# Kernel optimization log

Hardware: AMD Instinct MI355X
Metric: run time of the kernel (lower is better)

## Reference

```python
import jax, jax.numpy as jnp
import numpy as np

B, L, ENC_DIM, DEC_DIM, ATTN_DIM = 64, 2048, 1024, 1024, 512


def setup_inputs() -> dict:
    key = jax.random.key(0)
    ks = jax.random.split(key, 8)
    s_enc = 1.0 / np.sqrt(ENC_DIM)
    s_dec = 1.0 / np.sqrt(DEC_DIM)
    s_full = 1.0 / np.sqrt(ATTN_DIM)
    return {
        "encoder_out": jax.random.normal(ks[0], (B, L, ENC_DIM), jnp.float32),
        "decoder_hidden": jax.random.normal(ks[1], (B, DEC_DIM), jnp.float32),
        "We_w": jax.random.uniform(ks[2], (ENC_DIM, ATTN_DIM), jnp.float32, -s_enc, s_enc),
        "We_b": jax.random.uniform(ks[3], (ATTN_DIM,), jnp.float32, -s_enc, s_enc),
        "Wd_w": jax.random.uniform(ks[4], (DEC_DIM, ATTN_DIM), jnp.float32, -s_dec, s_dec),
        "Wd_b": jax.random.uniform(ks[5], (ATTN_DIM,), jnp.float32, -s_dec, s_dec),
        "Wf_w": jax.random.uniform(ks[6], (ATTN_DIM,), jnp.float32, -s_full, s_full),
        "Wf_b": jax.random.uniform(ks[7], (), jnp.float32, -s_full, s_full),
    }


def reference(encoder_out, decoder_hidden, We_w, We_b, Wd_w, Wd_b, Wf_w, Wf_b):
    # enc_attn: [B, L, A]; dec_attn: [B, A]
    enc_attn = jnp.einsum("ble,ea->bla", encoder_out, We_w) + We_b
    dec_attn = decoder_hidden @ Wd_w + Wd_b
    # additive score -> scalar per (B, L)
    hidden = jax.nn.relu(enc_attn + dec_attn[:, None, :])
    attn = jnp.einsum("bla,a->bl", hidden, Wf_w) + Wf_b
    alpha = jax.nn.softmax(attn, axis=1)  # over sequence dim
    weighted = jnp.einsum("ble,bl->be", encoder_out, alpha)
    return (weighted, alpha)
```

## Files before the change

kernel.cpp:

```cpp
#include <hip/hip_runtime.h>
#include <stdint.h>

#define B_BATCH 64
#define L_SEQ 2048
#define E_DIM 1024
#define A_DIM 512

typedef __attribute__((ext_vector_type(4))) float f32x4;
typedef __attribute__((ext_vector_type(8))) short bf16x8;
typedef __attribute__((ext_vector_type(2))) unsigned int u32x2;
typedef __attribute__((ext_vector_type(4))) unsigned int u32x4;

__device__ __forceinline__ unsigned short f2bf(float f) {
  unsigned u = __float_as_uint(f);
  u = (u + 0x7fffu + ((u >> 16) & 1u)) >> 16;
  return (unsigned short)u;
}

__device__ __forceinline__ u32x2 packbf(f32x4 v) {
  u32x2 r;
  r.x = (unsigned)f2bf(v.x) | ((unsigned)f2bf(v.y) << 16);
  r.y = (unsigned)f2bf(v.z) | ((unsigned)f2bf(v.w) << 16);
  return r;
}

#define CHUNKB 8192
#define ABUF (4 * CHUNKB)
#define BCHUNK 32768
#define BCOPY (32 * BCHUNK)

__global__ void prep_we_kernel(const float* __restrict__ We, char* __restrict__ wsB) {
  int t = blockIdx.x * 256 + threadIdx.x;
  int lane = t & 63;
  int colblk = (t >> 6) & 31;
  int step = t >> 11;
  int nl = lane & 15, g = lane >> 4;
  int col = colblk * 16 + nl;
  int k0 = step * 32 + 4 * g;
  unsigned q0 = (unsigned)f2bf(We[(size_t)(k0 + 0) * A_DIM + col]) |
                ((unsigned)f2bf(We[(size_t)(k0 + 1) * A_DIM + col]) << 16);
  unsigned q1 = (unsigned)f2bf(We[(size_t)(k0 + 2) * A_DIM + col]) |
                ((unsigned)f2bf(We[(size_t)(k0 + 3) * A_DIM + col]) << 16);
  unsigned q2 = (unsigned)f2bf(We[(size_t)(k0 + 16) * A_DIM + col]) |
                ((unsigned)f2bf(We[(size_t)(k0 + 17) * A_DIM + col]) << 16);
  unsigned q3 = (unsigned)f2bf(We[(size_t)(k0 + 18) * A_DIM + col]) |
                ((unsigned)f2bf(We[(size_t)(k0 + 19) * A_DIM + col]) << 16);
  u32x4 v; v.x = q0; v.y = q1; v.z = q2; v.w = q3;
#pragma unroll
  for (int c = 0; c < 8; ++c)
    *(u32x4*)(wsB + (size_t)c * BCOPY + (size_t)t * 16) = v;
}

__global__ void dec_comb_kernel(const float* __restrict__ dh, const float* __restrict__ Wd,
                                const float* __restrict__ Wdb, const float* __restrict__ Web,
                                float* __restrict__ dcomb) {
  __shared__ float sh[1024];
  const int b = blockIdx.x, tid = threadIdx.x;
  for (int i = tid; i < 1024; i += 128) sh[i] = dh[b * 1024 + i];
  __syncthreads();
  const int a = blockIdx.y * 128 + tid;
  float acc = Wdb[a] + Web[a];
#pragma unroll 4
  for (int e = 0; e < 1024; ++e) acc += sh[e] * Wd[(size_t)e * A_DIM + a];
  dcomb[b * A_DIM + a] = acc;
}

__global__ __launch_bounds__(512, 2) void score_gemm_kernel(
    const float* __restrict__ enc, const char* __restrict__ wsB,
    const float* __restrict__ dcomb, const float* __restrict__ wf,
    float* __restrict__ scoreOut) {
  __shared__ __align__(16) char smem[2 * ABUF];
  __shared__ float s_score[128];

  const int tid = threadIdx.x;
  const int lane = tid & 63;
  const int w = tid >> 6;
  const int g = lane >> 4;
  const int nl = lane & 15;
  const int gs = g ^ ((nl >> 1) & 3);

  const int row0 = (int)blockIdx.x * 128;
  const int bb = row0 >> 11;

  if (tid < 128) s_score[tid] = 0.0f;

  const float* encA = enc + (size_t)row0 * E_DIM;
  const int anl = nl * 64 + gs * 16;

  const int arow = tid >> 5;
  const int klq = tid & 31;
  const float* asrc = encA + (size_t)arow * E_DIM + klq * 4;
  const int aw_base = (klq >> 3) * CHUNKB + arow * 64 +
                      (((tid & 3) ^ ((arow >> 1) & 3)) << 4) + ((tid >> 2) & 1) * 8;

  const char* bsrc = wsB + (size_t)(blockIdx.x & 7) * BCOPY + (w * 4) * 1024 + lane * 16;

  f32x4 acc[8][4];
#pragma unroll
  for (int rt = 0; rt < 8; ++rt)
#pragma unroll
    for (int ct = 0; ct < 4; ++ct) {
      f32x4 z = {0.f, 0.f, 0.f, 0.f};
      acc[rt][ct] = z;
    }
  f32x4 ra[2][2];
  bf16x8 bfr[2][4];

#define LOAD_P(t_, s_)                                                          \
  do {                                                                          \
    ra[(s_) & 1][0] =                                                           \
        *(const f32x4*)(asrc + (size_t)(2 * (s_)) * 16 * E_DIM + (t_) * 128);   \
    ra[(s_) & 1][1] =                                                           \
        *(const f32x4*)(asrc + (size_t)(2 * (s_) + 1) * 16 * E_DIM + (t_) * 128); \
  } while (0)

#define LOAD_B(kcg_, sl_)                                                       \
  do {                                                                          \
    _Pragma("unroll") for (int ct = 0; ct < 4; ++ct) bfr[sl_][ct] =             \
        *(const bf16x8*)(bsrc + (size_t)(kcg_)*BCHUNK + ct * 1024);             \
  } while (0)

#define WRITE_P(s_, nb_)                                                        \
  do {                                                                          \
    *(u32x2*)(smem + (nb_) + aw_base + (2 * (s_)) * 1024) = packbf(ra[(s_) & 1][0]); \
    *(u32x2*)(smem + (nb_) + aw_base + (2 * (s_) + 1) * 1024) =                 \
        packbf(ra[(s_) & 1][1]);                                                \
  } while (0)

#define MFMA_CHUNK(cb_, s_, par_)                                               \
  do {                                                                          \
    bf16x8 afr[4];                                                              \
    _Pragma("unroll") for (int rt = 0; rt < 4; ++rt) afr[rt] =                  \
        *(const bf16x8*)(smem + (cb_) + (s_)*CHUNKB + anl + rt * 1024);         \
    __builtin_amdgcn_s_setprio(1);                                              \
    _Pragma("unroll") for (int rt = 0; rt < 4; ++rt)                            \
        _Pragma("unroll") for (int ct = 0; ct < 4; ++ct) acc[rt][ct] =          \
            __builtin_amdgcn_mfma_f32_16x16x32_bf16(afr[rt], bfr[par_][ct],     \
                                                    acc[rt][ct], 0, 0, 0);      \
    __builtin_amdgcn_s_setprio(0);                                              \
    _Pragma("unroll") for (int rt = 0; rt < 4; ++rt) afr[rt] =                  \
        *(const bf16x8*)(smem + (cb_) + (s_)*CHUNKB + anl + (rt + 4) * 1024);   \
    __builtin_amdgcn_s_setprio(1);                                              \
    _Pragma("unroll") for (int rt = 0; rt < 4; ++rt)                            \
        _Pragma("unroll") for (int ct = 0; ct < 4; ++ct) acc[rt + 4][ct] =      \
            __builtin_amdgcn_mfma_f32_16x16x32_bf16(afr[rt], bfr[par_][ct],     \
                                                    acc[rt + 4][ct], 0, 0, 0);  \
    __builtin_amdgcn_s_setprio(0);                                              \
  } while (0)

  LOAD_P(0, 0);
  LOAD_P(0, 1);
  asm volatile("s_waitcnt vmcnt(2)" ::: "memory");
  WRITE_P(0, 0);
  LOAD_P(0, 2);
  asm volatile("s_waitcnt vmcnt(2)" ::: "memory");
  WRITE_P(1, 0);
  LOAD_P(0, 3);
  asm volatile("s_waitcnt vmcnt(2)" ::: "memory");
  WRITE_P(2, 0);
  asm volatile("s_waitcnt vmcnt(0)" ::: "memory");
  WRITE_P(3, 0);
  LOAD_B(0, 0);
  asm volatile("s_waitcnt lgkmcnt(0)" ::: "memory");
  asm volatile("s_barrier" ::: "memory");

#pragma unroll 1
  for (int t = 0; t < 7; ++t) {
    const int cb = (t & 1) * ABUF;
    const int nb = cb ^ ABUF;
    LOAD_P(t + 1, 0);
    LOAD_B(4 * t + 1, 1);
    asm volatile("s_waitcnt vmcnt(6)" ::: "memory");
    MFMA_CHUNK(cb, 0, 0);
    LOAD_P(t + 1, 1);
    LOAD_B(4 * t + 2, 0);
    asm volatile("s_waitcnt vmcnt(6)" ::: "memory");
    WRITE_P(0, nb);
    MFMA_CHUNK(cb, 1, 1);
    LOAD_P(t + 1, 2);
    LOAD_B(4 * t + 3, 1);
    asm volatile("s_waitcnt vmcnt(6)" ::: "memory");
    WRITE_P(1, nb);
    MFMA_CHUNK(cb, 2, 0);
    LOAD_P(t + 1, 3);
    LOAD_B(4 * t + 4, 0);
    asm volatile("s_waitcnt vmcnt(4)" ::: "memory");
    WRITE_P(2, nb);
    WRITE_P(3, nb);
    MFMA_CHUNK(cb, 3, 1);
    asm volatile("s_waitcnt lgkmcnt(0)" ::: "memory");
    asm volatile("s_barrier" ::: "memory");
  }
  {
    const int cb = ABUF;
    LOAD_B(29, 1);
    asm volatile("s_waitcnt vmcnt(4)" ::: "memory");
    MFMA_CHUNK(cb, 0, 0);
    LOAD_B(30, 0);
    asm volatile("s_waitcnt vmcnt(4)" ::: "memory");
    MFMA_CHUNK(cb, 1, 1);
    LOAD_B(31, 1);
    asm volatile("s_waitcnt vmcnt(4)" ::: "memory");
    MFMA_CHUNK(cb, 2, 0);
    asm volatile("s_waitcnt vmcnt(0)" ::: "memory");
    MFMA_CHUNK(cb, 3, 1);
  }

#undef LOAD_P
#undef LOAD_B
#undef WRITE_P
#undef MFMA_CHUNK

  float db[4], wv[4];
#pragma unroll
  for (int ct = 0; ct < 4; ++ct) {
    int a = w * 64 + ct * 16 + nl;
    db[ct] = dcomb[bb * A_DIM + a];
    wv[ct] = wf[a];
  }
#pragma unroll
  for (int rt = 0; rt < 8; ++rt) {
#pragma unroll
    for (int r = 0; r < 4; ++r) {
      float p = 0.f;
#pragma unroll
      for (int ct = 0; ct < 4; ++ct) {
        float h = acc[rt][ct][r] + db[ct];
        h = h > 0.f ? h : 0.f;
        p += h * wv[ct];
      }
      p += __shfl_xor(p, 1);
      p += __shfl_xor(p, 2);
      p += __shfl_xor(p, 4);
      p += __shfl_xor(p, 8);
      if (nl == 0) atomicAdd(&s_score[rt * 16 + g * 4 + r], p);
    }
  }
  __syncthreads();
  if (tid < 128) scoreOut[row0 + tid] = s_score[tid];
}

__global__ void softmax_kernel(float* __restrict__ attn) {
  __shared__ float red[8];
  const int b = blockIdx.x, tid = threadIdx.x;
  float* p = attn + b * L_SEQ;
  float v[8];
  float m = -1e30f;
#pragma unroll
  for (int i = 0; i < 8; ++i) {
    v[i] = p[tid + i * 256];
    m = fmaxf(m, v[i]);
  }
#pragma unroll
  for (int off = 1; off < 64; off <<= 1) m = fmaxf(m, __shfl_xor(m, off));
  const int wid = tid >> 6;
  if ((tid & 63) == 0) red[wid] = m;
  __syncthreads();
  m = fmaxf(fmaxf(red[0], red[1]), fmaxf(red[2], red[3]));
  float s = 0.f;
#pragma unroll
  for (int i = 0; i < 8; ++i) {
    v[i] = __expf(v[i] - m);
    s += v[i];
  }
#pragma unroll
  for (int off = 1; off < 64; off <<= 1) s += __shfl_xor(s, off);
  __syncthreads();
  if ((tid & 63) == 0) red[4 + wid] = s;
  __syncthreads();
  const float inv = 1.0f / (red[4] + red[5] + red[6] + red[7]);
#pragma unroll
  for (int i = 0; i < 8; ++i) p[tid + i * 256] = v[i] * inv;
}

__global__ void weighted_part_kernel(const float* __restrict__ enc,
                                     const float* __restrict__ alpha,
                                     float* __restrict__ part) {
  __shared__ float sa[64];
  const int bid = blockIdx.x;
  const int b = bid >> 5, ls = bid & 31;
  const int tid = threadIdx.x;
  if (tid < 64) sa[tid] = alpha[b * L_SEQ + ls * 64 + tid];
  __syncthreads();
  const float* base = enc + ((size_t)(b * L_SEQ + ls * 64)) * E_DIM;
  f32x4 acc = {0.f, 0.f, 0.f, 0.f};
#pragma unroll 8
  for (int il = 0; il < 64; ++il) {
    f32x4 v = *(const f32x4*)(base + (size_t)il * E_DIM + tid * 4);
    float al = sa[il];
    acc.x += al * v.x;
    acc.y += al * v.y;
    acc.z += al * v.z;
    acc.w += al * v.w;
  }
  *(f32x4*)(part + (size_t)bid * E_DIM + tid * 4) = acc;
}

__global__ void weighted_reduce_kernel(const float* __restrict__ part,
                                       float* __restrict__ outW) {
  const int b = blockIdx.x, tid = threadIdx.x;
  const float* p = part + (size_t)b * 32 * E_DIM + tid * 4;
  f32x4 acc = {0.f, 0.f, 0.f, 0.f};
#pragma unroll 8
  for (int ls = 0; ls < 32; ++ls) {
    f32x4 v = *(const f32x4*)(p + (size_t)ls * E_DIM);
    acc.x += v.x;
    acc.y += v.y;
    acc.z += v.z;
    acc.w += v.w;
  }
  *(f32x4*)(outW + (size_t)b * E_DIM + tid * 4) = acc;
}

extern "C" void kernel_launch(void* const* d_in, const int* in_sizes, int n_in,
                              void* d_out, int out_size, void* d_ws, size_t ws_size,
                              hipStream_t stream) {
  const float* enc = (const float*)d_in[0];
  const float* dh = (const float*)d_in[1];
  const float* WeW = (const float*)d_in[2];
  const float* WeB = (const float*)d_in[3];
  const float* WdW = (const float*)d_in[4];
  const float* WdB = (const float*)d_in[5];
  const float* WfW = (const float*)d_in[6];

  float* out = (float*)d_out;
  float* outW = out;
  float* attn = out + B_BATCH * E_DIM;

  char* wsB = (char*)d_ws;
  float* dcomb = (float*)((char*)d_ws + 8 * (size_t)BCOPY);
  float* part = (float*)((char*)d_ws + 8 * (size_t)BCOPY +
                         (size_t)B_BATCH * A_DIM * sizeof(float));

  const size_t need = 8 * (size_t)BCOPY + (size_t)B_BATCH * A_DIM * sizeof(float) +
                      (size_t)B_BATCH * 32 * E_DIM * sizeof(float);
  if (ws_size < need) return;

  prep_we_kernel<<<256, 256, 0, stream>>>(WeW, wsB);
  dec_comb_kernel<<<dim3(B_BATCH, 4), 128, 0, stream>>>(dh, WdW, WdB, WeB, dcomb);
  score_gemm_kernel<<<(B_BATCH * L_SEQ) / 128, 512, 0, stream>>>(enc, wsB, dcomb, WfW, attn);
  softmax_kernel<<<B_BATCH, 256, 0, stream>>>(attn);
  weighted_part_kernel<<<B_BATCH * 32, 256, 0, stream>>>(enc, attn, part);
  weighted_reduce_kernel<<<B_BATCH, 256, 0, stream>>>(part, outW);
}
```

Baseline: 398.1 us.

## Halve score GEMM row tile to 64 and simplify to double-buffered loop

```diff
diff --git a/kernel.cpp b/kernel.cpp
--- a/kernel.cpp
+++ b/kernel.cpp
@@ -24,8 +24,8 @@
   return r;
 }
 
-#define CHUNKB 8192
-#define ABUF (4 * CHUNKB)
+#define CHUNKB 4096
+#define ABUF (2 * CHUNKB)
 #define BCHUNK 32768
 #define BCOPY (32 * BCHUNK)
 
@@ -65,12 +65,12 @@
   dcomb[b * A_DIM + a] = acc;
 }
 
-__global__ __launch_bounds__(512, 2) void score_gemm_kernel(
+__global__ __launch_bounds__(512, 4) void score_gemm_kernel(
     const float* __restrict__ enc, const char* __restrict__ wsB,
     const float* __restrict__ dcomb, const float* __restrict__ wf,
     float* __restrict__ scoreOut) {
   __shared__ __align__(16) char smem[2 * ABUF];
-  __shared__ float s_score[128];
+  __shared__ float s_score[64];
 
   const int tid = threadIdx.x;
   const int lane = tid & 63;
@@ -79,137 +79,87 @@
   const int nl = lane & 15;
   const int gs = g ^ ((nl >> 1) & 3);
 
-  const int row0 = (int)blockIdx.x * 128;
+  const int row0 = (int)blockIdx.x * 64;
   const int bb = row0 >> 11;
 
-  if (tid < 128) s_score[tid] = 0.0f;
+  if (tid < 64) s_score[tid] = 0.0f;
 
   const float* encA = enc + (size_t)row0 * E_DIM;
-  const int anl = nl * 64 + gs * 16;
-
-  const int arow = tid >> 5;
-  const int klq = tid & 31;
-  const float* asrc = encA + (size_t)arow * E_DIM + klq * 4;
-  const int aw_base = (klq >> 3) * CHUNKB + arow * 64 +
-                      (((tid & 3) ^ ((arow >> 1) & 3)) << 4) + ((tid >> 2) & 1) * 8;
+
+  int aoff[4];
+#pragma unroll
+  for (int rt = 0; rt < 4; ++rt) aoff[rt] = (rt * 16 + nl) * 64 + gs * 16;
+
+  const int ar = tid >> 3, ac = tid & 7;
+  const float* asrc = encA + (size_t)ar * E_DIM + ac * 4;
+  const int slot = (ac & 3) ^ ((ar >> 1) & 3);
+  const int aw0 = ar * 64 + slot * 16 + (ac >> 2) * 8;
+  const int aw1 = aw0 + CHUNKB;
 
   const char* bsrc = wsB + (size_t)(blockIdx.x & 7) * BCOPY + (w * 4) * 1024 + lane * 16;
 
-  f32x4 acc[8][4];
-#pragma unroll
-  for (int rt = 0; rt < 8; ++rt)
+  f32x4 acc[4][4];
+#pragma unroll
+  for (int rt = 0; rt < 4; ++rt)
 #pragma unroll
     for (int ct = 0; ct < 4; ++ct) {
       f32x4 z = {0.f, 0.f, 0.f, 0.f};
       acc[rt][ct] = z;
     }
-  f32x4 ra[2][2];
-  bf16x8 bfr[2][4];
-
-#define LOAD_P(t_, s_)                                                          \
-  do {                                                                          \
-    ra[(s_) & 1][0] =                                                           \
-        *(const f32x4*)(asrc + (size_t)(2 * (s_)) * 16 * E_DIM + (t_) * 128);   \
-    ra[(s_) & 1][1] =                                                           \
-        *(const f32x4*)(asrc + (size_t)(2 * (s_) + 1) * 16 * E_DIM + (t_) * 128); \
-  } while (0)
-
-#define LOAD_B(kcg_, sl_)                                                       \
-  do {                                                                          \
-    _Pragma("unroll") for (int ct = 0; ct < 4; ++ct) bfr[sl_][ct] =             \
-        *(const bf16x8*)(bsrc + (size_t)(kcg_)*BCHUNK + ct * 1024);             \
-  } while (0)
-
-#define WRITE_P(s_, nb_)                                                        \
-  do {                                                                          \
-    *(u32x2*)(smem + (nb_) + aw_base + (2 * (s_)) * 1024) = packbf(ra[(s_) & 1][0]); \
-    *(u32x2*)(smem + (nb_) + aw_base + (2 * (s_) + 1) * 1024) =                 \
-        packbf(ra[(s_) & 1][1]);                                                \
-  } while (0)
-
-#define MFMA_CHUNK(cb_, s_, par_)                                               \
-  do {                                                                          \
-    bf16x8 afr[4];                                                              \
-    _Pragma("unroll") for (int rt = 0; rt < 4; ++rt) afr[rt] =                  \
-        *(const bf16x8*)(smem + (cb_) + (s_)*CHUNKB + anl + rt * 1024);         \
-    __builtin_amdgcn_s_setprio(1);                                              \
-    _Pragma("unroll") for (int rt = 0; rt < 4; ++rt)                            \
-        _Pragma("unroll") for (int ct = 0; ct < 4; ++ct) acc[rt][ct] =          \
-            __builtin_amdgcn_mfma_f32_16x16x32_bf16(afr[rt], bfr[par_][ct],     \
-                                                    acc[rt][ct], 0, 0, 0);      \
-    __builtin_amdgcn_s_setprio(0);                                              \
-    _Pragma("unroll") for (int rt = 0; rt < 4; ++rt) afr[rt] =                  \
-        *(const bf16x8*)(smem + (cb_) + (s_)*CHUNKB + anl + (rt + 4) * 1024);   \
-    __builtin_amdgcn_s_setprio(1);                                              \
-    _Pragma("unroll") for (int rt = 0; rt < 4; ++rt)                            \
-        _Pragma("unroll") for (int ct = 0; ct < 4; ++ct) acc[rt + 4][ct] =      \
-            __builtin_amdgcn_mfma_f32_16x16x32_bf16(afr[rt], bfr[par_][ct],     \
-                                                    acc[rt + 4][ct], 0, 0, 0);  \
-    __builtin_amdgcn_s_setprio(0);                                              \
-  } while (0)
-
-  LOAD_P(0, 0);
-  LOAD_P(0, 1);
-  asm volatile("s_waitcnt vmcnt(2)" ::: "memory");
-  WRITE_P(0, 0);
-  LOAD_P(0, 2);
-  asm volatile("s_waitcnt vmcnt(2)" ::: "memory");
-  WRITE_P(1, 0);
-  LOAD_P(0, 3);
-  asm volatile("s_waitcnt vmcnt(2)" ::: "memory");
-  WRITE_P(2, 0);
-  asm volatile("s_waitcnt vmcnt(0)" ::: "memory");
-  WRITE_P(3, 0);
-  LOAD_B(0, 0);
-  asm volatile("s_waitcnt lgkmcnt(0)" ::: "memory");
-  asm volatile("s_barrier" ::: "memory");
+
+  {
+    f32x4 L0 = *(const f32x4*)(asrc);
+    f32x4 L1 = *(const f32x4*)(asrc + 32);
+    *(u32x2*)(smem + aw0) = packbf(L0);
+    *(u32x2*)(smem + aw1) = packbf(L1);
+  }
+  __syncthreads();
 
 #pragma unroll 1
-  for (int t = 0; t < 7; ++t) {
-    const int cb = (t & 1) * ABUF;
-    const int nb = cb ^ ABUF;
-    LOAD_P(t + 1, 0);
-    LOAD_B(4 * t + 1, 1);
-    asm volatile("s_waitcnt vmcnt(6)" ::: "memory");
-    MFMA_CHUNK(cb, 0, 0);
-    LOAD_P(t + 1, 1);
-    LOAD_B(4 * t + 2, 0);
-    asm volatile("s_waitcnt vmcnt(6)" ::: "memory");
-    WRITE_P(0, nb);
-    MFMA_CHUNK(cb, 1, 1);
-    LOAD_P(t + 1, 2);
-    LOAD_B(4 * t + 3, 1);
-    asm volatile("s_waitcnt vmcnt(6)" ::: "memory");
-    WRITE_P(1, nb);
-    MFMA_CHUNK(cb, 2, 0);
-    LOAD_P(t + 1, 3);
-    LOAD_B(4 * t + 4, 0);
-    asm volatile("s_waitcnt vmcnt(4)" ::: "memory");
-    WRITE_P(2, nb);
-    WRITE_P(3, nb);
-    MFMA_CHUNK(cb, 3, 1);
-    asm volatile("s_waitcnt lgkmcnt(0)" ::: "memory");
-    asm volatile("s_barrier" ::: "memory");
-  }
-  {
-    const int cb = ABUF;
-    LOAD_B(29, 1);
-    asm volatile("s_waitcnt vmcnt(4)" ::: "memory");
-    MFMA_CHUNK(cb, 0, 0);
-    LOAD_B(30, 0);
-    asm volatile("s_waitcnt vmcnt(4)" ::: "memory");
-    MFMA_CHUNK(cb, 1, 1);
-    LOAD_B(31, 1);
-    asm volatile("s_waitcnt vmcnt(4)" ::: "memory");
-    MFMA_CHUNK(cb, 2, 0);
-    asm volatile("s_waitcnt vmcnt(0)" ::: "memory");
-    MFMA_CHUNK(cb, 3, 1);
-  }
-
-#undef LOAD_P
-#undef LOAD_B
-#undef WRITE_P
-#undef MFMA_CHUNK
+  for (int t = 0; t < 16; ++t) {
+    const int cur = (t & 1) * ABUF;
+    const int nxt = cur ^ ABUF;
+    f32x4 L0, L1;
+    if (t < 15) {
+      L0 = *(const f32x4*)(asrc + (size_t)(t + 1) * 64);
+      L1 = *(const f32x4*)(asrc + (size_t)(t + 1) * 64 + 32);
+    }
+    {
+      bf16x8 bfr[4], afr[4];
+#pragma unroll
+      for (int ct = 0; ct < 4; ++ct)
+        bfr[ct] = *(const bf16x8*)(bsrc + (size_t)(2 * t) * BCHUNK + ct * 1024);
+#pragma unroll
+      for (int rt = 0; rt < 4; ++rt)
+        afr[rt] = *(const bf16x8*)(smem + cur + aoff[rt]);
+#pragma unroll
+      for (int rt = 0; rt < 4; ++rt)
+#pragma unroll
+        for (int ct = 0; ct < 4; ++ct)
+          acc[rt][ct] = __builtin_amdgcn_mfma_f32_16x16x32_bf16(afr[rt], bfr[ct],
+                                                                acc[rt][ct], 0, 0, 0);
+    }
+    {
+      bf16x8 bfr[4], afr[4];
+#pragma unroll
+      for (int ct = 0; ct < 4; ++ct)
+        bfr[ct] = *(const bf16x8*)(bsrc + (size_t)(2 * t + 1) * BCHUNK + ct * 1024);
+#pragma unroll
+      for (int rt = 0; rt < 4; ++rt)
+        afr[rt] = *(const bf16x8*)(smem + cur + CHUNKB + aoff[rt]);
+#pragma unroll
+      for (int rt = 0; rt < 4; ++rt)
+#pragma unroll
+        for (int ct = 0; ct < 4; ++ct)
+          acc[rt][ct] = __builtin_amdgcn_mfma_f32_16x16x32_bf16(afr[rt], bfr[ct],
+                                                                acc[rt][ct], 0, 0, 0);
+    }
+    if (t < 15) {
+      *(u32x2*)(smem + nxt + aw0) = packbf(L0);
+      *(u32x2*)(smem + nxt + aw1) = packbf(L1);
+    }
+    __syncthreads();
+  }
 
   float db[4], wv[4];
 #pragma unroll
@@ -219,7 +169,7 @@
     wv[ct] = wf[a];
   }
 #pragma unroll
-  for (int rt = 0; rt < 8; ++rt) {
+  for (int rt = 0; rt < 4; ++rt) {
 #pragma unroll
     for (int r = 0; r < 4; ++r) {
       float p = 0.f;
@@ -237,7 +187,7 @@
     }
   }
   __syncthreads();
-  if (tid < 128) scoreOut[row0 + tid] = s_score[tid];
+  if (tid < 64) scoreOut[row0 + tid] = s_score[tid];
 }
 
 __global__ void softmax_kernel(float* __restrict__ attn) {
@@ -338,7 +288,7 @@
 
   prep_we_kernel<<<256, 256, 0, stream>>>(WeW, wsB);
   dec_comb_kernel<<<dim3(B_BATCH, 4), 128, 0, stream>>>(dh, WdW, WdB, WeB, dcomb);
-  score_gemm_kernel<<<(B_BATCH * L_SEQ) / 128, 512, 0, stream>>>(enc, wsB, dcomb, WfW, attn);
+  score_gemm_kernel<<<(B_BATCH * L_SEQ) / 64, 512, 0, stream>>>(enc, wsB, dcomb, WfW, attn);
   softmax_kernel<<<B_BATCH, 256, 0, stream>>>(attn);
   weighted_part_kernel<<<B_BATCH * 32, 256, 0, stream>>>(enc, attn, part);
   weighted_reduce_kernel<<<B_BATCH, 256, 0, stream>>>(part, outW);
```

Measured after the change: 408.7 us. +2.7%, slower.
